# Optimization experiments

Measured on AMD Instinct MI355X. Metric: run time of the kernel, lower is better.

The kernel has to match this reference:

```python
import jax, jax.numpy as jnp
import numpy as np

B, R, IMG_DIM, TAG_DIM = 256, 36, 2048, 768
BOX_LEN = 15
POS_EMBED = 200
POS_SIZE = 16 * 16 + 1  # 257
EMBED_SIZE = 1024
EPS_NORM = 1e-8
EPS_ATTN = 1e-6


def setup_inputs() -> dict:
    key = jax.random.key(0)
    ks = jax.random.split(key, 8)
    images = jax.random.normal(ks[0], (B, R, IMG_DIM), dtype=jnp.float32)
    images_tag = jax.random.normal(ks[1], (B, R, TAG_DIM), dtype=jnp.float32)
    # boxes: first 15 entries are integer position indices, last 15 are weights
    box_idx = jax.random.randint(ks[2], (B, R, BOX_LEN), 0, POS_SIZE).astype(jnp.float32)
    box_w = jax.random.uniform(ks[3], (B, R, BOX_LEN), dtype=jnp.float32)
    boxes = jnp.concatenate([box_idx, box_w], axis=-1)  # [B,R,30]
    # parameters (xavier-uniform-like for linears, normal for embedding)
    pos_emb = jax.random.normal(ks[4], (POS_SIZE, POS_EMBED), dtype=jnp.float32)
    fan = (IMG_DIM + TAG_DIM) + POS_EMBED
    r1 = np.sqrt(6.0) / np.sqrt(fan)
    attn_W = jax.random.uniform(ks[5], (POS_EMBED, IMG_DIM + TAG_DIM), dtype=jnp.float32, minval=-r1, maxval=r1)
    fc_in = IMG_DIM + POS_EMBED + TAG_DIM
    r2 = np.sqrt(6.0) / np.sqrt(fc_in + EMBED_SIZE)
    fc_W = jax.random.uniform(ks[6], (EMBED_SIZE, fc_in), dtype=jnp.float32, minval=-r2, maxval=r2)
    fc_b = jnp.zeros((EMBED_SIZE,), dtype=jnp.float32)
    return {"images": images, "images_tag": images_tag, "boxes": boxes,
            "pos_emb": pos_emb, "attn_W": attn_W, "fc_W": fc_W, "fc_b": fc_b}


def reference(images, images_tag, boxes, pos_emb, attn_W, fc_W, fc_b):
    half = boxes.shape[2] // 2  # 15
    idx = boxes[..., :half].astype(jnp.int32)        # [B,R,15] position indices
    box_w = boxes[..., half:]                        # [B,R,15] weights
    img_tag = jnp.concatenate([images, images_tag], axis=-1)  # [B,R,2816]
    box_emb = pos_emb[idx]                           # [B,R,15,200]
    # posi_attn (vectorized over batch instead of python loop)
    region = jnp.einsum('brd,ed->bre', img_tag, attn_W)        # [B,R,200]
    scores = jnp.einsum('bre,brke->brk', region, box_emb)      # [B,R,15]
    attn = jax.nn.softmax(jnp.tanh(scores), axis=-1)
    attn = attn * box_w
    attn = attn / (jnp.sum(attn, axis=-1, keepdims=True) + EPS_ATTN)
    box_feat = jnp.einsum('brk,brke->bre', attn, box_emb)      # [B,R,200]
    # original uses .data -> detached attention output
    box_feat = jax.lax.stop_gradient(box_feat)
    image_position = jnp.concatenate([images, box_feat, images_tag], axis=-1)  # [B,R,3016]
    features = jnp.einsum('brd,ed->bre', image_position, fc_W) + fc_b
    norm = jnp.sqrt(jnp.sum(features ** 2, axis=-1, keepdims=True)) + EPS_NORM
    return features / norm
```

## Files before the change

### kernel.cpp

```cpp
#include <hip/hip_runtime.h>


#define M_TOT 9216
#define K1    2816
#define K2    3072
#define ES    1024

typedef __attribute__((ext_vector_type(8))) short bf16x8;
typedef __attribute__((ext_vector_type(4))) float floatx4;

static __device__ __forceinline__ unsigned short f2bf(float f) {
    unsigned int u = __float_as_uint(f);
    u += 0x7fffu + ((u >> 16) & 1u);
    return (unsigned short)(u >> 16);
}

static __device__ __forceinline__ uint4 pack8(const float4 f0, const float4 f1) {
    uint4 pk;
    pk.x = (unsigned)f2bf(f0.x) | ((unsigned)f2bf(f0.y) << 16);
    pk.y = (unsigned)f2bf(f0.z) | ((unsigned)f2bf(f0.w) << 16);
    pk.z = (unsigned)f2bf(f1.x) | ((unsigned)f2bf(f1.y) << 16);
    pk.w = (unsigned)f2bf(f1.z) | ((unsigned)f2bf(f1.w) << 16);
    return pk;
}

static __device__ __forceinline__ void cvt8(const float* __restrict__ g,
                                            unsigned short* __restrict__ d) {
    *(uint4*)d = pack8(*(const float4*)g, *(const float4*)(g + 4));
}

static __device__ __forceinline__ void gl16(const void* g, const void* l) {
    __builtin_amdgcn_global_load_lds(
        (const __attribute__((address_space(1))) unsigned int*)g,
        (__attribute__((address_space(3))) unsigned int*)(unsigned int)(unsigned long long)l,
        16, 0, 0);
}

#define NC_WF  (1024 * 384)
#define NC_WA  ( 208 * 352)
__global__ __launch_bounds__(256) void k_prep_w(
    const float* __restrict__ attn_W,
    const float* __restrict__ fc_W,
    unsigned short* __restrict__ Wa,
    unsigned short* __restrict__ Wf)
{
    const int u = blockIdx.x * 256 + threadIdx.x;
    uint4 z; z.x = z.y = z.z = z.w = 0u;
    if (u < NC_WF) {
        const int r = u / 384;
        const int dc = (u - r * 384) * 8;
        unsigned short* d = Wf + (long)r * K2 + dc;
        if (dc < 2248)      cvt8(fc_W + (long)r * 3016 + dc, d);
        else if (dc < 2304) *(uint4*)d = z;
        else                cvt8(fc_W + (long)r * 3016 + (dc - 56), d);
    } else if (u < NC_WF + NC_WA) {
        const int v = u - NC_WF;
        const int r = v / 352;
        const int c = (v - r * 352) * 8;
        if (r < 200) cvt8(attn_W + (long)r * K1 + c, Wa + (long)r * K1 + c);
        else         *(uint4*)(Wa + (long)r * K1 + c) = z;
    }
}

__global__ __launch_bounds__(256, 4) void k_gemm1(
    const float* __restrict__ images,
    const float* __restrict__ tag,
    const unsigned short* __restrict__ Wa,
    unsigned short* __restrict__ Abf,
    float* __restrict__ regP)
{
    __shared__ __align__(16) unsigned short ldsA[64 * 64];
    __shared__ __align__(16) unsigned short ldsB[208 * 64];

    const int t = threadIdx.x;
    const int lane = t & 63;
    const int w = t >> 6;
    const int quad = lane >> 4;
    const int ln15 = lane & 15;
    const int x7 = ln15 & 7;
    const int bid = blockIdx.x;
    const int m0 = (bid >> 2) * 64;
    const int kh = bid & 3;
    const int kbase = kh * 704;
    const int lrow = lane >> 3;
    const int schunk = (lane & 7) ^ lrow;

    const int rA = t >> 3;
    const int gA = t & 7;
    const int aslot0 = rA * 64 + ((gA ^ (rA & 7)) << 3);
    const int aslot1 = (rA + 32) * 64 + ((gA ^ (rA & 7)) << 3);

    floatx4 acc[13] = {};
    float4 p0a, p0b, p1a, p1b;

    {
        const float* s0 = (kbase < 2048)
            ? images + (long)(m0 + rA) * 2048 + kbase + gA * 8
            : tag + (long)(m0 + rA) * 768 + (kbase - 2048) + gA * 8;
        const float* s1 = (kbase < 2048)
            ? images + (long)(m0 + rA + 32) * 2048 + kbase + gA * 8
            : tag + (long)(m0 + rA + 32) * 768 + (kbase - 2048) + gA * 8;
        p0a = *(const float4*)s0; p0b = *(const float4*)(s0 + 4);
        p1a = *(const float4*)s1; p1b = *(const float4*)(s1 + 4);
    }

    for (int kt = 0; kt < 11; ++kt) {
        const int kb = kbase + kt * 64;
        {
            const uint4 k0 = pack8(p0a, p0b);
            const uint4 k1 = pack8(p1a, p1b);
            *(uint4*)&ldsA[aslot0] = k0;
            *(uint4*)&ldsA[aslot1] = k1;
            const int acol = kb + ((kb >= 2048) ? 256 : 0);
            *(uint4*)(Abf + (long)(m0 + rA) * K2 + acol + gA * 8) = k0;
            *(uint4*)(Abf + (long)(m0 + rA + 32) * K2 + acol + gA * 8) = k1;
        }
#pragma unroll
        for (int i = 0; i < 7; ++i) {
            const int u = w + i * 4;
            if (u < 26)
                gl16(Wa + (long)(u * 8 + lrow) * K1 + kb + schunk * 8, ldsB + u * 512);
        }
        if (kt < 10) {
            const int kn = kb + 64;
            const float* s0 = (kn < 2048)
                ? images + (long)(m0 + rA) * 2048 + kn + gA * 8
                : tag + (long)(m0 + rA) * 768 + (kn - 2048) + gA * 8;
            const float* s1 = (kn < 2048)
                ? images + (long)(m0 + rA + 32) * 2048 + kn + gA * 8
                : tag + (long)(m0 + rA + 32) * 768 + (kn - 2048) + gA * 8;
            p0a = *(const float4*)s0; p0b = *(const float4*)(s0 + 4);
            p1a = *(const float4*)s1; p1b = *(const float4*)(s1 + 4);
        }
        __syncthreads();
#pragma unroll
        for (int s = 0; s < 2; ++s) {
            const int g = s * 4 + quad;
            const int co = (g ^ x7) << 3;
            const bf16x8 a = *(const bf16x8*)&ldsA[(w * 16 + ln15) * 64 + co];
#pragma unroll
            for (int j = 0; j < 13; ++j) {
                const bf16x8 b = *(const bf16x8*)&ldsB[(j * 16 + ln15) * 64 + co];
                acc[j] = __builtin_amdgcn_mfma_f32_16x16x32_bf16(a, b, acc[j], 0, 0, 0);
            }
        }
        __syncthreads();
    }

#pragma unroll
    for (int j = 0; j < 13; ++j)
#pragma unroll
        for (int r = 0; r < 4; ++r)
            atomicAdd(&regP[(long)(m0 + w * 16 + quad * 4 + r) * 208 + j * 16 + ln15],
                      acc[j][r]);
}

__global__ __launch_bounds__(256, 4) void k_attn(
    const float* __restrict__ regP,
    const float* __restrict__ boxes,
    const float* __restrict__ pos_emb,
    unsigned short* __restrict__ Abf)
{
    const int t = threadIdx.x;
    const int lane = t & 63;
    const int w = t >> 6;
    const int m = blockIdx.x * 4 + w;

    const float* r0 = regP + (long)m * 208;
    float rv[4];
#pragma unroll
    for (int c = 0; c < 4; ++c) {
        const int e = lane + c * 64;
        rv[c] = (e < 200) ? r0[e] : 0.0f;
    }
    const float* bx = boxes + (long)m * 30;
    int idx[15]; float bw[15], sc_[15];
#pragma unroll
    for (int k = 0; k < 15; ++k) {
        int ii = (int)bx[k];
        idx[k] = (ii < 0) ? 0 : (ii > 256 ? 256 : ii);
        bw[k] = bx[15 + k];
    }
#pragma unroll
    for (int k = 0; k < 15; ++k) {
        const float* em = pos_emb + (long)idx[k] * 200;
        float p = 0.0f;
#pragma unroll
        for (int c = 0; c < 4; ++c) {
            const int e = lane + c * 64;
            if (e < 200) p += rv[c] * em[e];
        }
        for (int off = 32; off; off >>= 1) p += __shfl_xor(p, off, 64);
        sc_[k] = p;
    }
    float mx = -1e30f;
#pragma unroll
    for (int k = 0; k < 15; ++k) { sc_[k] = tanhf(sc_[k]); mx = fmaxf(mx, sc_[k]); }
    float Z = 0.0f, den = 0.0f, pk[15];
#pragma unroll
    for (int k = 0; k < 15; ++k) { pk[k] = __expf(sc_[k] - mx); Z += pk[k]; }
#pragma unroll
    for (int k = 0; k < 15; ++k) { pk[k] *= bw[k]; den += pk[k]; }
    den += 1e-6f * Z;
    const float inv = 1.0f / den;
    unsigned short* bo = Abf + (long)m * K2 + 2048;
#pragma unroll
    for (int c = 0; c < 4; ++c) {
        const int e = lane + c * 64;
        float o = 0.0f;
        if (e < 200) {
#pragma unroll
            for (int k = 0; k < 15; ++k) o += pk[k] * pos_emb[(long)idx[k] * 200 + e];
            o *= inv;
        }
        bo[e] = f2bf(o);
    }
}

__global__ __launch_bounds__(384, 3) void k_gemm2(
    const unsigned short* __restrict__ Abf,
    const unsigned short* __restrict__ Wf,
    float* __restrict__ dout)
{
    __shared__ __align__(16) unsigned short ldsA[144 * 64];
    __shared__ __align__(16) unsigned short ldsB[128 * 64];
    const int t = threadIdx.x;
    const int lane = t & 63;
    const int w = t >> 6;
    const int quad = lane >> 4;
    const int ln15 = lane & 15;
    const int x7 = ln15 & 7;
    const int nx = blockIdx.x & 7;
    const int mx = blockIdx.x >> 3;
    const int m0 = mx * 144;
    const int n0 = nx * 128;
    const int lrow = lane >> 3;
    const int schunk = (lane & 7) ^ lrow;
    const int wm = (w % 3) * 48;
    const int wn = (w / 3) * 64;

    floatx4 acc[3][4] = {};

    for (int kt = 0; kt < 48; ++kt) {
        const int kb = kt * 64;
#pragma unroll
        for (int i = 0; i < 6; ++i) {
            const int u = w + i * 6;
            if (u < 18)
                gl16(Abf + (long)(m0 + u * 8 + lrow) * K2 + kb + schunk * 8, ldsA + u * 512);
            else if (u < 34)
                gl16(Wf + (long)(n0 + (u - 18) * 8 + lrow) * K2 + kb + schunk * 8,
                     ldsB + (u - 18) * 512);
        }
        __syncthreads();
#pragma unroll
        for (int s = 0; s < 2; ++s) {
            const int g = s * 4 + quad;
            const int co = (g ^ x7) << 3;
            bf16x8 a[3], b[4];
#pragma unroll
            for (int i = 0; i < 3; ++i)
                a[i] = *(const bf16x8*)&ldsA[(wm + i * 16 + ln15) * 64 + co];
#pragma unroll
            for (int j = 0; j < 4; ++j)
                b[j] = *(const bf16x8*)&ldsB[(wn + j * 16 + ln15) * 64 + co];
#pragma unroll
            for (int i = 0; i < 3; ++i)
#pragma unroll
                for (int j = 0; j < 4; ++j)
                    acc[i][j] = __builtin_amdgcn_mfma_f32_16x16x32_bf16(a[i], b[j], acc[i][j], 0, 0, 0);
        }
        __syncthreads();
    }
#pragma unroll
    for (int i = 0; i < 3; ++i)
#pragma unroll
        for (int j = 0; j < 4; ++j) {
            const int row = m0 + wm + i * 16 + quad * 4;
            const int col = n0 + wn + j * 16 + ln15;
#pragma unroll
            for (int r = 0; r < 4; ++r)
                dout[(long)(row + r) * ES + col] = acc[i][j][r];
        }
}

__global__ __launch_bounds__(256) void k_norm(
    float* __restrict__ dout,
    const float* __restrict__ bias)
{
    __shared__ float red[4];
    const int m = blockIdx.x;
    const int t = threadIdx.x;
    float* f = dout + (long)m * ES + t * 4;
    float4 v = *(const float4*)f;
    const float4 bs = *(const float4*)(bias + t * 4);
    v.x += bs.x; v.y += bs.y; v.z += bs.z; v.w += bs.w;
    float ss = v.x * v.x + v.y * v.y + v.z * v.z + v.w * v.w;
    for (int off = 32; off; off >>= 1) ss += __shfl_xor(ss, off, 64);
    if ((t & 63) == 0) red[t >> 6] = ss;
    __syncthreads();
    const float total = red[0] + red[1] + red[2] + red[3];
    const float inv = 1.0f / (sqrtf(total) + 1e-8f);
    float4 o;
    o.x = v.x * inv; o.y = v.y * inv; o.z = v.z * inv; o.w = v.w * inv;
    *(float4*)f = o;
}

extern "C" void kernel_launch(void* const* d_in, const int* in_sizes, int n_in,
                              void* d_out, int out_size, void* d_ws, size_t ws_size,
                              hipStream_t stream) {
    const float* images  = (const float*)d_in[0];
    const float* tag     = (const float*)d_in[1];
    const float* boxes   = (const float*)d_in[2];
    const float* pos_emb = (const float*)d_in[3];
    const float* attn_W  = (const float*)d_in[4];
    const float* fc_W    = (const float*)d_in[5];
    const float* fc_b    = (const float*)d_in[6];
    float* out = (float*)d_out;

    unsigned short* Abf = (unsigned short*)d_ws;
    unsigned short* Wf  = Abf + (size_t)M_TOT * K2;
    unsigned short* Wa  = Wf  + (size_t)ES * K2;
    float* regP = (float*)(Wa + (size_t)208 * K1);

    k_prep_w<<<1822, 256, 0, stream>>>(attn_W, fc_W, Wa, Wf);
    hipMemsetAsync(regP, 0, (size_t)M_TOT * 208 * sizeof(float), stream);
    k_gemm1 <<<576, 256, 0, stream>>>(images, tag, Wa, Abf, regP);
    k_attn  <<<2304, 256, 0, stream>>>(regP, boxes, pos_emb, Abf);
    k_gemm2 <<<512, 384, 0, stream>>>(Abf, Wf, out);
    k_norm  <<<M_TOT, 256, 0, stream>>>(out, fc_b);
}
```

Before: 307.5 us.

## Move A fp32-to-bf16 conversion into separate prep kernel, fold regP memset

Adds a standalone kernel that converts images and tags to bf16 in the Abf workspace, so gemm1 now streams its A tiles straight into LDS with async global_load_lds instead of loading fp32 into registers, packing, and writing both LDS and global. The regP zeroing is folded into the weight-prep kernel, which removes the separate memset. The cost is an extra full pass over the A matrix (an fp32 read plus a bf16 write, then a bf16 re-read in gemm1) and one more kernel launch, in exchange for a simpler, fully asynchronous gemm1 load path.

```diff
diff --git a/kernel.cpp b/kernel.cpp
--- a/kernel.cpp
+++ b/kernel.cpp
@@ -15,18 +15,16 @@
     return (unsigned short)(u >> 16);
 }
 
-static __device__ __forceinline__ uint4 pack8(const float4 f0, const float4 f1) {
+static __device__ __forceinline__ void cvt8(const float* __restrict__ g,
+                                            unsigned short* __restrict__ d) {
+    const float4 f0 = *(const float4*)g;
+    const float4 f1 = *(const float4*)(g + 4);
     uint4 pk;
     pk.x = (unsigned)f2bf(f0.x) | ((unsigned)f2bf(f0.y) << 16);
     pk.y = (unsigned)f2bf(f0.z) | ((unsigned)f2bf(f0.w) << 16);
     pk.z = (unsigned)f2bf(f1.x) | ((unsigned)f2bf(f1.y) << 16);
     pk.w = (unsigned)f2bf(f1.z) | ((unsigned)f2bf(f1.w) << 16);
-    return pk;
-}
-
-static __device__ __forceinline__ void cvt8(const float* __restrict__ g,
-                                            unsigned short* __restrict__ d) {
-    *(uint4*)d = pack8(*(const float4*)g, *(const float4*)(g + 4));
+    *(uint4*)d = pk;
 }
 
 static __device__ __forceinline__ void gl16(const void* g, const void* l) {
@@ -36,13 +34,31 @@
         16, 0, 0);
 }
 
+#define NC_ABF (9216 * 352)
+__global__ __launch_bounds__(256) void k_prep_a(
+    const float* __restrict__ images,
+    const float* __restrict__ tag,
+    unsigned short* __restrict__ Abf)
+{
+    const int stride = gridDim.x * 256;
+    for (int u = blockIdx.x * 256 + threadIdx.x; u < NC_ABF; u += stride) {
+        const int m = u / 352;
+        const int c = u - m * 352;
+        if (c < 256) cvt8(images + (long)m * 2048 + c * 8, Abf + (long)m * K2 + c * 8);
+        else         cvt8(tag + (long)m * 768 + (c - 256) * 8,
+                          Abf + (long)m * K2 + 2304 + (c - 256) * 8);
+    }
+}
+
 #define NC_WF  (1024 * 384)
 #define NC_WA  ( 208 * 352)
+#define NC_RP  (9216 * 208 / 4)
 __global__ __launch_bounds__(256) void k_prep_w(
     const float* __restrict__ attn_W,
     const float* __restrict__ fc_W,
     unsigned short* __restrict__ Wa,
-    unsigned short* __restrict__ Wf)
+    unsigned short* __restrict__ Wf,
+    float* __restrict__ regP)
 {
     const int u = blockIdx.x * 256 + threadIdx.x;
     uint4 z; z.x = z.y = z.z = z.w = 0u;
@@ -59,14 +75,14 @@
         const int c = (v - r * 352) * 8;
         if (r < 200) cvt8(attn_W + (long)r * K1 + c, Wa + (long)r * K1 + c);
         else         *(uint4*)(Wa + (long)r * K1 + c) = z;
+    } else if (u < NC_WF + NC_WA + NC_RP) {
+        ((uint4*)regP)[u - NC_WF - NC_WA] = z;
     }
 }
 
 __global__ __launch_bounds__(256, 4) void k_gemm1(
-    const float* __restrict__ images,
-    const float* __restrict__ tag,
+    const unsigned short* __restrict__ Abf,
     const unsigned short* __restrict__ Wa,
-    unsigned short* __restrict__ Abf,
     float* __restrict__ regP)
 {
     __shared__ __align__(16) unsigned short ldsA[64 * 64];
@@ -85,52 +101,21 @@
     const int lrow = lane >> 3;
     const int schunk = (lane & 7) ^ lrow;
 
-    const int rA = t >> 3;
-    const int gA = t & 7;
-    const int aslot0 = rA * 64 + ((gA ^ (rA & 7)) << 3);
-    const int aslot1 = (rA + 32) * 64 + ((gA ^ (rA & 7)) << 3);
-
     floatx4 acc[13] = {};
-    float4 p0a, p0b, p1a, p1b;
-
-    {
-        const float* s0 = (kbase < 2048)
-            ? images + (long)(m0 + rA) * 2048 + kbase + gA * 8
-            : tag + (long)(m0 + rA) * 768 + (kbase - 2048) + gA * 8;
-        const float* s1 = (kbase < 2048)
-            ? images + (long)(m0 + rA + 32) * 2048 + kbase + gA * 8
-            : tag + (long)(m0 + rA + 32) * 768 + (kbase - 2048) + gA * 8;
-        p0a = *(const float4*)s0; p0b = *(const float4*)(s0 + 4);
-        p1a = *(const float4*)s1; p1b = *(const float4*)(s1 + 4);
-    }
 
     for (int kt = 0; kt < 11; ++kt) {
         const int kb = kbase + kt * 64;
-        {
-            const uint4 k0 = pack8(p0a, p0b);
-            const uint4 k1 = pack8(p1a, p1b);
-            *(uint4*)&ldsA[aslot0] = k0;
-            *(uint4*)&ldsA[aslot1] = k1;
-            const int acol = kb + ((kb >= 2048) ? 256 : 0);
-            *(uint4*)(Abf + (long)(m0 + rA) * K2 + acol + gA * 8) = k0;
-            *(uint4*)(Abf + (long)(m0 + rA + 32) * K2 + acol + gA * 8) = k1;
-        }
-#pragma unroll
-        for (int i = 0; i < 7; ++i) {
+        const int acol = kb + ((kb >= 2048) ? 256 : 0);
+#pragma unroll
+        for (int i = 0; i < 9; ++i) {
             const int u = w + i * 4;
-            if (u < 26)
-                gl16(Wa + (long)(u * 8 + lrow) * K1 + kb + schunk * 8, ldsB + u * 512);
-        }
-        if (kt < 10) {
-            const int kn = kb + 64;
-            const float* s0 = (kn < 2048)
-                ? images + (long)(m0 + rA) * 2048 + kn + gA * 8
-                : tag + (long)(m0 + rA) * 768 + (kn - 2048) + gA * 8;
-            const float* s1 = (kn < 2048)
-                ? images + (long)(m0 + rA + 32) * 2048 + kn + gA * 8
-                : tag + (long)(m0 + rA + 32) * 768 + (kn - 2048) + gA * 8;
-            p0a = *(const float4*)s0; p0b = *(const float4*)(s0 + 4);
-            p1a = *(const float4*)s1; p1b = *(const float4*)(s1 + 4);
+            if (u < 8) {
+                gl16(Abf + (long)(m0 + u * 8 + lrow) * K2 + acol + schunk * 8,
+                     ldsA + u * 512);
+            } else if (u < 34) {
+                gl16(Wa + (long)((u - 8) * 8 + lrow) * K1 + kb + schunk * 8,
+                     ldsB + (u - 8) * 512);
+            }
         }
         __syncthreads();
 #pragma unroll
@@ -323,9 +308,10 @@
     unsigned short* Wa  = Wf  + (size_t)ES * K2;
     float* regP = (float*)(Wa + (size_t)208 * K1);
 
-    k_prep_w<<<1822, 256, 0, stream>>>(attn_W, fc_W, Wa, Wf);
-    hipMemsetAsync(regP, 0, (size_t)M_TOT * 208 * sizeof(float), stream);
-    k_gemm1 <<<576, 256, 0, stream>>>(images, tag, Wa, Abf, regP);
+    k_prep_a<<<4096, 256, 0, stream>>>(images, tag, Abf);
+    k_prep_w<<<(NC_WF + NC_WA + NC_RP + 255) / 256, 256, 0, stream>>>(
+        attn_W, fc_W, Wa, Wf, (float*)regP);
+    k_gemm1 <<<576, 256, 0, stream>>>(Abf, Wa, regP);
     k_attn  <<<2304, 256, 0, stream>>>(regP, boxes, pos_emb, Abf);
     k_gemm2 <<<512, 384, 0, stream>>>(Abf, Wf, out);
     k_norm  <<<M_TOT, 256, 0, stream>>>(out, fc_b);
```

Result: no change. 311.0 us (+1.1%).
